# Optimization experiments

Hardware: AMD Instinct MI355X
Metric: run time of the kernel (lower is better)

## Reference

```python
import jax, jax.numpy as jnp
import numpy as np

B, S, D_DIM = 32, 512, 1024

def setup_inputs() -> dict:
    key = jax.random.key(0)
    k1, k2, k3, k4 = jax.random.split(key, 4)
    return {
        "D": jax.random.normal(k1, (B, S, D_DIM), dtype=jnp.float32),
        "H": jax.random.normal(k2, (B, S, D_DIM), dtype=jnp.float32),
        # learned params: U is (d+1, d) (xavier-style scale), W is (2d+1,)
        # (original inits W to zeros; we use small random values so the linear
        #  term is exercised — same math either way)
        "U": jax.random.normal(k3, (D_DIM + 1, D_DIM), dtype=jnp.float32) * 0.02,
        "W": jax.random.normal(k4, (2 * D_DIM + 1,), dtype=jnp.float32) * 0.02,
    }

def reference(D, H, U, W):
    # D, H: [B, S, d]; U: [d+1, d]; W: [2d+1]
    d = H.shape[-1]
    ones = jnp.ones(D.shape[:2] + (1,), dtype=D.dtype)
    Daug = jnp.concatenate([D, ones], axis=-1)              # [B, S, d+1]
    # bilinear term: v.U.u  -> [B, Sx, Sy]
    bil = jnp.einsum('bxi,ij,byj->bxy', Daug, U, H)
    # linear term W . concat(D_aug, H): algebraically split — avoids the
    # O(B*S*S*2d) concatenated intermediate of the original implementation
    lin = (Daug @ W[:d + 1])[:, :, None] + (H @ W[d + 1:])[:, None, :]
    return bil + lin
```

## Files before the change

### kernel.cpp

```cpp
#include <hip/hip_runtime.h>


#define D_DIM 1024
#define ROWS 16384

typedef float floatx4 __attribute__((ext_vector_type(4)));
typedef __bf16 bf16x8 __attribute__((ext_vector_type(8)));

__device__ inline unsigned short f2bf(float f) {
  unsigned int u = __builtin_bit_cast(unsigned int, f);
  u = (u + 0x7FFFu + ((u >> 16) & 1u)) >> 16;
  return (unsigned short)u;
}

__device__ inline void async_load16(const void* g, void* l) {
  __builtin_amdgcn_global_load_lds(
      (const __attribute__((address_space(1))) void*)g,
      (__attribute__((address_space(3))) void*)l, 16, 0, 0);
}

__global__ __launch_bounds__(256) void cast_rows_kernel(
    const float* __restrict__ D, const float* __restrict__ H,
    const float* __restrict__ W, const float* __restrict__ Wh,
    unsigned short* __restrict__ Dbf, unsigned short* __restrict__ Hbf,
    float* __restrict__ linD, float* __restrict__ linH) {
  __shared__ float lds[16][256];
  int t = threadIdx.x;
  bool isH = blockIdx.x >= 1024;
  int r0 = (blockIdx.x & 1023) * 16;
  const float* src = (isH ? H : D) + (size_t)r0 * D_DIM;
  unsigned short* dst = (isH ? Hbf : Dbf) + (size_t)r0 * D_DIM;
  float4 w4 = ((const float4*)(isH ? Wh : W))[t];

  #pragma unroll
  for (int i = 0; i < 16; ++i) {
    float4 v = ((const float4*)src)[i * 256 + t];
    lds[i][t] = v.x * w4.x + v.y * w4.y + v.z * w4.z + v.w * w4.w;
    ushort4 o;
    o.x = f2bf(v.x); o.y = f2bf(v.y); o.z = f2bf(v.z); o.w = f2bf(v.w);
    ((ushort4*)dst)[i * 256 + t] = o;
  }
  __syncthreads();

  int wave = t >> 6, l = t & 63;
  float* lin = isH ? linH : linD;
  float bias = isH ? 0.f : W[D_DIM];
  #pragma unroll
  for (int c = 0; c < 4; ++c) {
    int r = wave * 4 + c;
    float4 p = *(const float4*)&lds[r][4 * l];
    float s = p.x + p.y + p.z + p.w;
    #pragma unroll
    for (int off = 32; off > 0; off >>= 1) s += __shfl_down(s, off, 64);
    if (l == 0) lin[r0 + r] = s + bias;
  }
}

__global__ __launch_bounds__(256) void transU_kernel(
    const float* __restrict__ U, const float* __restrict__ W,
    unsigned short* __restrict__ Ut, float* __restrict__ Wh) {
  if (blockIdx.x == 0 && blockIdx.y == 0) {
    #pragma unroll
    for (int i = 0; i < 4; ++i)
      Wh[threadIdx.x + 256 * i] = W[D_DIM + 1 + threadIdx.x + 256 * i];
  }
  __shared__ float tile[32][33];
  int n0 = blockIdx.x * 32;
  int k0 = blockIdx.y * 32;
  int t = threadIdx.x;
  int tr = t >> 5, tc = t & 31;
  #pragma unroll
  for (int i = 0; i < 32; i += 8)
    tile[tr + i][tc] = U[(size_t)(k0 + tr + i) * D_DIM + n0 + tc];
  __syncthreads();
  #pragma unroll
  for (int i = 0; i < 32; i += 8)
    Ut[(size_t)(n0 + tr + i) * D_DIM + k0 + tc] = f2bf(tile[tc][tr + i]);
}

__device__ inline void gemm_core_swz(
    const unsigned short* __restrict__ A, const unsigned short* __restrict__ Bt,
    int m0, int n0, unsigned short* As, unsigned short* Bs,
    floatx4 (&acc)[4][4]) {
  const int K = D_DIM;
  int tid = threadIdx.x;
  int l = tid & 63, wave = tid >> 6;
  int quad = l >> 4, lrow = l & 15;
  int wm = wave >> 1, wn = wave & 1;

  int srow = 8 * wave + (l >> 3);
  int sq = (l & 7) ^ (l >> 3);
  const unsigned short* gA = A + (size_t)(m0 + srow) * K + sq * 8;
  const unsigned short* gB = Bt + (size_t)(n0 + srow) * K + sq * 8;

  int rl = lrow & 7, gofs = lrow >> 3;
  int baseA = wm * 512 + gofs * 64 + rl * 8;
  int baseB = wn * 512 + gofs * 64 + rl * 8;

  for (int k0 = 0; k0 < K; k0 += 64) {
    __syncthreads();
    #pragma unroll
    for (int j = 0; j < 4; ++j) {
      async_load16(gA + (size_t)(32 * j) * K + k0, As + (j * 256 + tid) * 8);
      async_load16(gB + (size_t)(32 * j) * K + k0, Bs + (j * 256 + tid) * 8);
    }
    __syncthreads();
    #pragma unroll
    for (int s = 0; s < 2; ++s) {
      int xq = (s * 4 + quad) ^ rl;
      bf16x8 a[4], b[4];
      #pragma unroll
      for (int mt = 0; mt < 4; ++mt)
        a[mt] = *(const bf16x8*)(As + (baseA + mt * 128 + xq) * 8);
      #pragma unroll
      for (int nt = 0; nt < 4; ++nt)
        b[nt] = *(const bf16x8*)(Bs + (baseB + nt * 128 + xq) * 8);
      #pragma unroll
      for (int mt = 0; mt < 4; ++mt)
        #pragma unroll
        for (int nt = 0; nt < 4; ++nt)
          acc[mt][nt] = __builtin_amdgcn_mfma_f32_16x16x32_bf16(
              a[mt], b[nt], acc[mt][nt], 0, 0, 0);
    }
  }
}

__global__ __launch_bounds__(256) void gemm1_kernel(
    const unsigned short* __restrict__ A,
    const unsigned short* __restrict__ Bt,
    const float* __restrict__ Ubias,
    unsigned short* __restrict__ T) {
  __shared__ __align__(16) unsigned short As[128 * 64];
  __shared__ __align__(16) unsigned short Bs[128 * 64];
  int m0 = blockIdx.x * 128, n0 = blockIdx.y * 128;
  int tid = threadIdx.x;
  int lane = tid & 63, wave = tid >> 6;
  int quad = lane >> 4, lrow = lane & 15;
  int wm = wave >> 1, wn = wave & 1;

  floatx4 acc[4][4] = {};
  gemm_core_swz(A, Bt, m0, n0, As, Bs, acc);

  #pragma unroll
  for (int mt = 0; mt < 4; ++mt)
    #pragma unroll
    for (int nt = 0; nt < 4; ++nt) {
      int row = m0 + wm * 64 + mt * 16 + quad * 4;
      int col = n0 + wn * 64 + nt * 16 + lrow;
      float bias = Ubias[col];
      #pragma unroll
      for (int rr = 0; rr < 4; ++rr)
        T[(size_t)(row + rr) * D_DIM + col] = f2bf(acc[mt][nt][rr] + bias);
    }
}

__global__ __launch_bounds__(256) void gemm2_kernel(
    const unsigned short* __restrict__ Tg,
    const unsigned short* __restrict__ Hbf,
    const float* __restrict__ linD, const float* __restrict__ linH,
    float* __restrict__ out) {
  __shared__ __align__(16) unsigned short As[128 * 64];
  __shared__ __align__(16) unsigned short Bs[128 * 64];
  int b = blockIdx.x;
  int t = blockIdx.y;
  int m0 = (t >> 2) * 128, n0 = (t & 3) * 128;
  const unsigned short* A = Tg + (size_t)b * 512 * D_DIM;
  const unsigned short* Bt = Hbf + (size_t)b * 512 * D_DIM;
  int tid = threadIdx.x;
  int lane = tid & 63, wave = tid >> 6;
  int quad = lane >> 4, lrow = lane & 15;
  int wm = wave >> 1, wn = wave & 1;

  floatx4 acc[4][4] = {};
  gemm_core_swz(A, Bt, m0, n0, As, Bs, acc);

  #pragma unroll
  for (int mt = 0; mt < 4; ++mt)
    #pragma unroll
    for (int nt = 0; nt < 4; ++nt) {
      int row = m0 + wm * 64 + mt * 16 + quad * 4;
      int col = n0 + wn * 64 + nt * 16 + lrow;
      float lh = linH[b * 512 + col];
      #pragma unroll
      for (int rr = 0; rr < 4; ++rr) {
        float v = acc[mt][nt][rr] + linD[b * 512 + row + rr] + lh;
        out[((size_t)b * 512 + row + rr) * 512 + col] = v;
      }
    }
}

extern "C" void kernel_launch(void* const* d_in, const int* in_sizes, int n_in,
                              void* d_out, int out_size, void* d_ws, size_t ws_size,
                              hipStream_t stream) {
  const float* D = (const float*)d_in[0];
  const float* H = (const float*)d_in[1];
  const float* U = (const float*)d_in[2];
  const float* W = (const float*)d_in[3];
  float* out = (float*)d_out;

  char* ws = (char*)d_ws;
  unsigned short* Dbf = (unsigned short*)ws; ws += (size_t)ROWS * D_DIM * 2;
  unsigned short* Hbf = (unsigned short*)ws; ws += (size_t)ROWS * D_DIM * 2;
  unsigned short* Tbf = (unsigned short*)ws; ws += (size_t)ROWS * D_DIM * 2;
  unsigned short* Ut  = (unsigned short*)ws; ws += (size_t)D_DIM * D_DIM * 2;
  float* linD = (float*)ws;                  ws += (size_t)ROWS * 4;
  float* linH = (float*)ws;                  ws += (size_t)ROWS * 4;
  float* Wh   = (float*)ws;                  ws += (size_t)D_DIM * 4;

  transU_kernel<<<dim3(32, 32), 256, 0, stream>>>(U, W, Ut, Wh);
  cast_rows_kernel<<<dim3(2048), 256, 0, stream>>>(D, H, W, Wh, Dbf, Hbf, linD, linH);
  gemm1_kernel<<<dim3(128, 8), 256, 0, stream>>>(Dbf, Ut, U + (size_t)D_DIM * D_DIM, Tbf);
  gemm2_kernel<<<dim3(32, 16), 256, 0, stream>>>(Tbf, Hbf, linD, linH, out);
}
```

Before: 232.5 us.

## Fuse fp32-to-bf16 casting and linear terms into GEMM tile loads

Removes the separate cast kernel. The GEMMs now read fp32 D/H directly, convert them to bf16 in registers while storing into swizzled LDS, and accumulate the W dot products along the way. This avoids writing and re-reading the bf16 copies of D and H. In exchange, the fp32 operand is reread once per N-tile (8x for D in gemm1, 4x for H in gemm2) with synchronous loads instead of async LDS loads. gemm2 also recomputes linH redundantly in each tile.

```diff
diff --git a/kernel.cpp b/kernel.cpp
--- a/kernel.cpp
+++ b/kernel.cpp
@@ -6,6 +6,7 @@
 
 typedef float floatx4 __attribute__((ext_vector_type(4)));
 typedef __bf16 bf16x8 __attribute__((ext_vector_type(8)));
+typedef __bf16 bf16x4 __attribute__((ext_vector_type(4)));
 
 __device__ inline unsigned short f2bf(float f) {
   unsigned int u = __builtin_bit_cast(unsigned int, f);
@@ -17,43 +18,6 @@
   __builtin_amdgcn_global_load_lds(
       (const __attribute__((address_space(1))) void*)g,
       (__attribute__((address_space(3))) void*)l, 16, 0, 0);
-}
-
-__global__ __launch_bounds__(256) void cast_rows_kernel(
-    const float* __restrict__ D, const float* __restrict__ H,
-    const float* __restrict__ W, const float* __restrict__ Wh,
-    unsigned short* __restrict__ Dbf, unsigned short* __restrict__ Hbf,
-    float* __restrict__ linD, float* __restrict__ linH) {
-  __shared__ float lds[16][256];
-  int t = threadIdx.x;
-  bool isH = blockIdx.x >= 1024;
-  int r0 = (blockIdx.x & 1023) * 16;
-  const float* src = (isH ? H : D) + (size_t)r0 * D_DIM;
-  unsigned short* dst = (isH ? Hbf : Dbf) + (size_t)r0 * D_DIM;
-  float4 w4 = ((const float4*)(isH ? Wh : W))[t];
-
-  #pragma unroll
-  for (int i = 0; i < 16; ++i) {
-    float4 v = ((const float4*)src)[i * 256 + t];
-    lds[i][t] = v.x * w4.x + v.y * w4.y + v.z * w4.z + v.w * w4.w;
-    ushort4 o;
-    o.x = f2bf(v.x); o.y = f2bf(v.y); o.z = f2bf(v.z); o.w = f2bf(v.w);
-    ((ushort4*)dst)[i * 256 + t] = o;
-  }
-  __syncthreads();
-
-  int wave = t >> 6, l = t & 63;
-  float* lin = isH ? linH : linD;
-  float bias = isH ? 0.f : W[D_DIM];
-  #pragma unroll
-  for (int c = 0; c < 4; ++c) {
-    int r = wave * 4 + c;
-    float4 p = *(const float4*)&lds[r][4 * l];
-    float s = p.x + p.y + p.z + p.w;
-    #pragma unroll
-    for (int off = 32; off > 0; off >>= 1) s += __shfl_down(s, off, 64);
-    if (l == 0) lin[r0 + r] = s + bias;
-  }
 }
 
 __global__ __launch_bounds__(256) void transU_kernel(
@@ -78,9 +42,13 @@
     Ut[(size_t)(n0 + tr + i) * D_DIM + k0 + tc] = f2bf(tile[tc][tr + i]);
 }
 
-__device__ inline void gemm_core_swz(
-    const unsigned short* __restrict__ A, const unsigned short* __restrict__ Bt,
-    int m0, int n0, unsigned short* As, unsigned short* Bs,
+template <bool F32_IS_A>
+__device__ inline void gemm_core_mixed(
+    const unsigned short* __restrict__ Ga,
+    const float* __restrict__ Gf,
+    const float* __restrict__ Wv,
+    bool do_lin, float (&part)[8],
+    unsigned short* As, unsigned short* Bs,
     floatx4 (&acc)[4][4]) {
   const int K = D_DIM;
   int tid = threadIdx.x;
@@ -88,21 +56,40 @@
   int quad = l >> 4, lrow = l & 15;
   int wm = wave >> 1, wn = wave & 1;
 
+  unsigned short* Sasync = F32_IS_A ? Bs : As;
+  unsigned short* Sf32   = F32_IS_A ? As : Bs;
+
   int srow = 8 * wave + (l >> 3);
   int sq = (l & 7) ^ (l >> 3);
-  const unsigned short* gA = A + (size_t)(m0 + srow) * K + sq * 8;
-  const unsigned short* gB = Bt + (size_t)(n0 + srow) * K + sq * 8;
+  const unsigned short* gasync = Ga + (size_t)srow * K + sq * 8;
 
   int rl = lrow & 7, gofs = lrow >> 3;
   int baseA = wm * 512 + gofs * 64 + rl * 8;
   int baseB = wn * 512 + gofs * 64 + rl * 8;
 
+  int qi = tid & 15;
+  const float* gf = Gf + (size_t)(tid >> 4) * K + qi * 4;
+
   for (int k0 = 0; k0 < K; k0 += 64) {
     __syncthreads();
     #pragma unroll
-    for (int j = 0; j < 4; ++j) {
-      async_load16(gA + (size_t)(32 * j) * K + k0, As + (j * 256 + tid) * 8);
-      async_load16(gB + (size_t)(32 * j) * K + k0, Bs + (j * 256 + tid) * 8);
+    for (int j = 0; j < 4; ++j)
+      async_load16(gasync + (size_t)(32 * j) * K + k0, Sasync + (j * 256 + tid) * 8);
+    float4 v[8];
+    #pragma unroll
+    for (int i = 0; i < 8; ++i)
+      v[i] = *(const float4*)(gf + (size_t)(16 * i) * K + k0);
+    float4 wq;
+    if (do_lin) wq = *(const float4*)(Wv + k0 + qi * 4);
+    #pragma unroll
+    for (int i = 0; i < 8; ++i) {
+      if (do_lin)
+        part[i] += v[i].x * wq.x + v[i].y * wq.y + v[i].z * wq.z + v[i].w * wq.w;
+      int row = 16 * i + (tid >> 4);
+      int q = qi >> 1, half = qi & 1;
+      int c = (row >> 3) * 64 + (row & 7) * 8 + (q ^ (row & 7));
+      bf16x4 o = { (__bf16)v[i].x, (__bf16)v[i].y, (__bf16)v[i].z, (__bf16)v[i].w };
+      *(bf16x4*)(Sf32 + c * 8 + half * 4) = o;
     }
     __syncthreads();
     #pragma unroll
@@ -126,10 +113,12 @@
 }
 
 __global__ __launch_bounds__(256) void gemm1_kernel(
-    const unsigned short* __restrict__ A,
-    const unsigned short* __restrict__ Bt,
+    const float* __restrict__ Df,
+    const unsigned short* __restrict__ Ut,
     const float* __restrict__ Ubias,
-    unsigned short* __restrict__ T) {
+    const float* __restrict__ W,
+    unsigned short* __restrict__ T,
+    float* __restrict__ linD) {
   __shared__ __align__(16) unsigned short As[128 * 64];
   __shared__ __align__(16) unsigned short Bs[128 * 64];
   int m0 = blockIdx.x * 128, n0 = blockIdx.y * 128;
@@ -137,9 +126,12 @@
   int lane = tid & 63, wave = tid >> 6;
   int quad = lane >> 4, lrow = lane & 15;
   int wm = wave >> 1, wn = wave & 1;
-
+  bool do_lin = (blockIdx.y == 0);
+
+  float part[8] = {};
   floatx4 acc[4][4] = {};
-  gemm_core_swz(A, Bt, m0, n0, As, Bs, acc);
+  gemm_core_mixed<true>(Ut + (size_t)n0 * D_DIM, Df + (size_t)m0 * D_DIM,
+                        W, do_lin, part, As, Bs, acc);
 
   #pragma unroll
   for (int mt = 0; mt < 4; ++mt)
@@ -152,27 +144,59 @@
       for (int rr = 0; rr < 4; ++rr)
         T[(size_t)(row + rr) * D_DIM + col] = f2bf(acc[mt][nt][rr] + bias);
     }
+
+  if (do_lin) {
+    __syncthreads();
+    float* red = (float*)As;
+    #pragma unroll
+    for (int i = 0; i < 8; ++i)
+      red[(16 * i + (tid >> 4)) * 16 + (tid & 15)] = part[i];
+    __syncthreads();
+    if (tid < 128) {
+      float s = 0.f;
+      #pragma unroll
+      for (int j = 0; j < 16; ++j) s += red[tid * 16 + j];
+      linD[m0 + tid] = s + W[D_DIM];
+    }
+  }
 }
 
 __global__ __launch_bounds__(256) void gemm2_kernel(
     const unsigned short* __restrict__ Tg,
-    const unsigned short* __restrict__ Hbf,
-    const float* __restrict__ linD, const float* __restrict__ linH,
+    const float* __restrict__ Hf,
+    const float* __restrict__ Wh,
+    const float* __restrict__ linD,
     float* __restrict__ out) {
   __shared__ __align__(16) unsigned short As[128 * 64];
   __shared__ __align__(16) unsigned short Bs[128 * 64];
+  __shared__ float linh_s[128];
   int b = blockIdx.x;
   int t = blockIdx.y;
   int m0 = (t >> 2) * 128, n0 = (t & 3) * 128;
-  const unsigned short* A = Tg + (size_t)b * 512 * D_DIM;
-  const unsigned short* Bt = Hbf + (size_t)b * 512 * D_DIM;
   int tid = threadIdx.x;
   int lane = tid & 63, wave = tid >> 6;
   int quad = lane >> 4, lrow = lane & 15;
   int wm = wave >> 1, wn = wave & 1;
 
+  float part[8] = {};
   floatx4 acc[4][4] = {};
-  gemm_core_swz(A, Bt, m0, n0, As, Bs, acc);
+  gemm_core_mixed<false>(Tg + ((size_t)b * 512 + m0) * D_DIM,
+                         Hf + ((size_t)b * 512 + n0) * D_DIM,
+                         Wh, true, part, As, Bs, acc);
+
+  __syncthreads();
+  float* red = (float*)Bs;
+  #pragma unroll
+  for (int i = 0; i < 8; ++i)
+    red[(16 * i + (tid >> 4)) * 16 + (tid & 15)] = part[i];
+  __syncthreads();
+  if (tid < 128) {
+    float s = 0.f;
+    #pragma unroll
+    for (int j = 0; j < 16; ++j) s += red[tid * 16 + j];
+    linh_s[tid] = s;
+  }
+  __syncthreads();
 
   #pragma unroll
   for (int mt = 0; mt < 4; ++mt)
@@ -180,7 +204,7 @@
     for (int nt = 0; nt < 4; ++nt) {
       int row = m0 + wm * 64 + mt * 16 + quad * 4;
       int col = n0 + wn * 64 + nt * 16 + lrow;
-      float lh = linH[b * 512 + col];
+      float lh = linh_s[wn * 64 + nt * 16 + lrow];
       #pragma unroll
       for (int rr = 0; rr < 4; ++rr) {
         float v = acc[mt][nt][rr] + linD[b * 512 + row + rr] + lh;
@@ -199,16 +223,12 @@
   float* out = (float*)d_out;
 
   char* ws = (char*)d_ws;
-  unsigned short* Dbf = (unsigned short*)ws; ws += (size_t)ROWS * D_DIM * 2;
-  unsigned short* Hbf = (unsigned short*)ws; ws += (size_t)ROWS * D_DIM * 2;
   unsigned short* Tbf = (unsigned short*)ws; ws += (size_t)ROWS * D_DIM * 2;
   unsigned short* Ut  = (unsigned short*)ws; ws += (size_t)D_DIM * D_DIM * 2;
   float* linD = (float*)ws;                  ws += (size_t)ROWS * 4;
-  float* linH = (float*)ws;                  ws += (size_t)ROWS * 4;
   float* Wh   = (float*)ws;                  ws += (size_t)D_DIM * 4;
 
   transU_kernel<<<dim3(32, 32), 256, 0, stream>>>(U, W, Ut, Wh);
-  cast_rows_kernel<<<dim3(2048), 256, 0, stream>>>(D, H, W, Wh, Dbf, Hbf, linD, linH);
-  gemm1_kernel<<<dim3(128, 8), 256, 0, stream>>>(Dbf, Ut, U + (size_t)D_DIM * D_DIM, Tbf);
-  gemm2_kernel<<<dim3(32, 16), 256, 0, stream>>>(Tbf, Hbf, linD, linH, out);
-}
+  gemm1_kernel<<<dim3(128, 8), 256, 0, stream>>>(D, Ut, U + (size_t)D_DIM * D_DIM, W, Tbf, linD);
+  gemm2_kernel<<<dim3(32, 16), 256, 0, stream>>>(Tbf, H, Wh, linD, out);
+}
```

New measurement: 226.3 us. 2.7% less time.
